# Optimization experiments

Hardware: AMD Instinct MI355X
Metric: run time of the kernel (lower is better)

The kernel has to match this reference:

```python
import jax, jax.numpy as jnp
import numpy as np
from jax import lax

EPS = 1e-6
D_MODEL = 2048
N_HEADS = 32
D_STATE = 64
HEADDIM = D_MODEL // N_HEADS  # 64, d_inner = expand*d_model = 2048
D_CONV = 4
INTER = 5504


def rmsnorm(x, w, eps=EPS):
    v = jnp.mean(jnp.square(x.astype(jnp.float32)), axis=-1, keepdims=True)
    return (x.astype(jnp.float32) * lax.rsqrt(v + eps)).astype(x.dtype) * w


def ssm_scan(x, dt, Bm, Cm):
    # x: (b,l,h,p) unscaled; dt: (b,l,h); Bm,Cm: (b,l,h,n)
    # DiscreteMamba2: h_t = exp(-dt_t) h_{t-1} + x_t (x) B_t ; y_t = h_t . C_t
    # (mamba_chunk_scan is called with x/dt and A=-1, so dt*(x/dt)=x)
    a = jnp.exp(-dt)  # (b,l,h)
    b, l, h, p = x.shape
    n = Bm.shape[-1]

    def step(hst, inp):
        a_t, x_t, B_t, C_t = inp
        hst = a_t[..., None, None] * hst + jnp.einsum('bhp,bhn->bhpn', x_t, B_t)
        y = jnp.einsum('bhpn,bhn->bhp', hst, C_t)
        return hst, y

    h0 = jnp.zeros((b, h, p, n), dtype=x.dtype)
    xs = (jnp.moveaxis(a, 1, 0), jnp.moveaxis(x, 1, 0),
          jnp.moveaxis(Bm, 1, 0), jnp.moveaxis(Cm, 1, 0))
    _, ys = lax.scan(step, h0, xs)
    return jnp.moveaxis(ys, 0, 1)  # (b,l,h,p)


def setup_inputs() -> dict:
    key = jax.random.key(0)
    ks = jax.random.split(key, 8)
    s = 0.02
    d_inner = D_MODEL
    conv_dim = d_inner + 2 * N_HEADS * D_STATE  # 6144
    d_in_proj = 2 * d_inner + 2 * N_HEADS * D_STATE + N_HEADS  # 8224
    return {
        'hidden_states': jax.random.normal(ks[0], (2, 2048, D_MODEL), jnp.float32),
        'attention_mask': jnp.ones((2, 2048), jnp.float32),
        'in_proj_w': jax.random.normal(ks[1], (d_in_proj, D_MODEL), jnp.float32) * s,
        'conv_w': jax.random.normal(ks[2], (conv_dim, 1, D_CONV), jnp.float32) * s,
        'conv_b': jnp.zeros((conv_dim,), jnp.float32),
        'z_bias': jnp.zeros((d_inner,), jnp.float32),
        'D': jnp.ones((N_HEADS,), jnp.float32),
        'out_proj_w': jax.random.normal(ks[3], (D_MODEL, d_inner), jnp.float32) * s,
        'ln1_w': jnp.ones((D_MODEL,), jnp.float32),
        'ln2_w': jnp.ones((D_MODEL,), jnp.float32),
        'gate_w': jax.random.normal(ks[4], (INTER, D_MODEL), jnp.float32) * s,
        'up_w': jax.random.normal(ks[5], (INTER, D_MODEL), jnp.float32) * s,
        'down_w': jax.random.normal(ks[6], (D_MODEL, INTER), jnp.float32) * s,
    }


def reference(hidden_states, attention_mask, in_proj_w, conv_w, conv_b, z_bias,
              D, out_proj_w, ln1_w, ln2_w, gate_w, up_w, down_w):
    b, l, d_model = hidden_states.shape
    d_inner = z_bias.shape[0]
    h_heads = D.shape[0]
    conv_dim = conv_w.shape[0]
    d_state = (conv_dim - d_inner) // (2 * h_heads)
    headdim = d_inner // h_heads

    residual = hidden_states
    h = rmsnorm(hidden_states, ln1_w)
    h = h * attention_mask[..., None]

    # --- DiscreteMamba2 mixer ---
    zxbcdt = jnp.einsum('bld,ed->ble', h, in_proj_w)
    z = zxbcdt[..., :d_inner]
    xBC = zxbcdt[..., d_inner:d_inner + conv_dim]
    A_log = zxbcdt[..., d_inner + conv_dim:]  # (b,l,h)

    # causal depthwise conv (activation = identity)
    xc = jnp.pad(jnp.swapaxes(xBC, 1, 2), ((0, 0), (0, 0), (conv_w.shape[-1] - 1, 0)))
    xBC = lax.conv_general_dilated(xc, conv_w, (1,), 'VALID',
                                   dimension_numbers=('NCH', 'OIH', 'NCH'),
                                   feature_group_count=conv_dim)
    xBC = jnp.swapaxes(xBC + conv_b[None, :, None], 1, 2)  # (b,l,conv_dim)

    x = xBC[..., :d_inner].reshape(b, l, h_heads, headdim)
    Bm = xBC[..., d_inner:d_inner + h_heads * d_state].reshape(b, l, h_heads, d_state)
    Cm = xBC[..., d_inner + h_heads * d_state:].reshape(b, l, h_heads, d_state)

    dt = jax.nn.softplus(A_log)  # (b,l,h)
    y = ssm_scan(x, dt, Bm, Cm)
    y = y + D[None, None, :, None] * x  # D skip uses unscaled x
    y = y.reshape(b, l, d_inner)

    gated = y * jax.nn.silu(z + z_bias)
    mixer_out = jnp.einsum('bld,ed->ble', gated, out_proj_w)

    h = mixer_out + residual
    residual2 = h
    h = rmsnorm(h, ln2_w)
    mlp = jnp.einsum('bli,di->bld',
                     jax.nn.silu(jnp.einsum('bld,id->bli', h, gate_w)) *
                     jnp.einsum('bld,id->bli', h, up_w),
                     down_w)
    return residual2 + mlp
```

## Files before the change

kernel.cpp:

```cpp
#include <hip/hip_runtime.h>
#include <math.h>

typedef __bf16 bf16_t;
typedef __attribute__((ext_vector_type(8))) __bf16 bf16x8;
typedef __attribute__((ext_vector_type(4))) float f32x4;

#define D_MODEL   2048
#define L_SEQ     2048
#define BATCH     2
#define NTOK      4096
#define N_HEADS   32
#define D_STATE   64
#define HEADDIM   64
#define D_INNER   2048
#define CONV_DIM  6144
#define D_IN_PROJ 8224
#define INTER     5504
#define QCHUNK    128
#define KCHUNKS   16

__device__ __forceinline__ void gld_lds16(const void* g, void* l) {
    __builtin_amdgcn_global_load_lds(
        (const __attribute__((address_space(1))) unsigned int*)g,
        (__attribute__((address_space(3))) unsigned int*)l, 16, 0, 0);
}

__device__ __forceinline__ int xcd_swizzle(int orig, int nwg) {
    int qx = nwg >> 3, rx = nwg & 7;
    int xcd = orig & 7, l8 = orig >> 3;
    return (xcd < rx ? xcd * (qx + 1) : rx * (qx + 1) + (xcd - rx) * qx) + l8;
}

__global__ __launch_bounds__(256) void cvt_kernel(
    const float* __restrict__ s, bf16_t* __restrict__ d, int n8)
{
    int i = blockIdx.x * 256 + threadIdx.x;
    if (i >= n8) return;
    const float4* s4 = (const float4*)s;
    float4 a = s4[2 * i], b = s4[2 * i + 1];
    bf16x8 r;
    r[0] = (bf16_t)a.x; r[1] = (bf16_t)a.y; r[2] = (bf16_t)a.z; r[3] = (bf16_t)a.w;
    r[4] = (bf16_t)b.x; r[5] = (bf16_t)b.y; r[6] = (bf16_t)b.z; r[7] = (bf16_t)b.w;
    ((bf16x8*)d)[i] = r;
}

__global__ __launch_bounds__(256) void rmsnorm_kernel(
    const float* __restrict__ x, const float* __restrict__ w,
    const float* __restrict__ mask, bf16_t* __restrict__ out)
{
    __shared__ float red[4];
    __shared__ float sinv;
    int row = blockIdx.x;
    const float* xr = x + (size_t)row * D_MODEL;
    float xv[8];
    float ss = 0.f;
#pragma unroll
    for (int i = 0; i < 8; ++i) {
        float v = xr[threadIdx.x + 256 * i];
        xv[i] = v;
        ss += v * v;
    }
    for (int off = 32; off >= 1; off >>= 1) ss += __shfl_down(ss, off, 64);
    int lane = threadIdx.x & 63, wv = threadIdx.x >> 6;
    if (lane == 0) red[wv] = ss;
    __syncthreads();
    if (threadIdx.x == 0) {
        float t = red[0] + red[1] + red[2] + red[3];
        sinv = rsqrtf(t / (float)D_MODEL + 1e-6f);
    }
    __syncthreads();
    float s = sinv;
    float m = mask ? mask[row] : 1.f;
    bf16_t* orow = out + (size_t)row * D_MODEL;
#pragma unroll
    for (int i = 0; i < 8; ++i) {
        int c = threadIdx.x + 256 * i;
        orow[c] = (bf16_t)(xv[i] * s * w[c] * m);
    }
}

template <bool RES, typename OT>
__global__ __launch_bounds__(256) void gemm_bt(
    const bf16_t* __restrict__ X, const bf16_t* __restrict__ W,
    const float* __restrict__ R, OT* __restrict__ O,
    int N, int K, int ldo)
{
    __shared__ __attribute__((aligned(16))) bf16_t As[128 * 32];
    __shared__ __attribute__((aligned(16))) bf16_t Bs[128 * 32];

    int tid = threadIdx.x;
    int ny = gridDim.y;
    int wg = xcd_swizzle(blockIdx.x + gridDim.x * blockIdx.y, gridDim.x * ny);
    int m0 = (wg % ny) * 128;
    int n0 = (wg / ny) * 128;

    f32x4 acc[4][4] = {};

    int lane = tid & 63;
    int wv = tid >> 6;
    int wm = (wv >> 1) * 64, wn = (wv & 1) * 64;
    int lm = lane & 15, lq = lane >> 4;

    int srow = tid >> 2;
    int scol = (tid & 3) * 8;
    const bf16_t* Xp0 = X + (size_t)(m0 + srow) * K + scol;
    const bf16_t* Xp1 = X + (size_t)(m0 + 64 + srow) * K + scol;
    int wr0 = n0 + srow;      if (wr0 > N - 1) wr0 = N - 1;
    int wr1 = n0 + 64 + srow; if (wr1 > N - 1) wr1 = N - 1;
    const bf16_t* Wp0 = W + (size_t)wr0 * K + scol;
    const bf16_t* Wp1 = W + (size_t)wr1 * K + scol;
    bf16_t* lA0 = &As[tid * 8];
    bf16_t* lA1 = &As[2048 + tid * 8];
    bf16_t* lB0 = &Bs[tid * 8];
    bf16_t* lB1 = &Bs[2048 + tid * 8];

    for (int k0 = 0; k0 < K; k0 += 32) {
        __syncthreads();
        gld_lds16(Xp0 + k0, lA0);
        gld_lds16(Xp1 + k0, lA1);
        gld_lds16(Wp0 + k0, lB0);
        gld_lds16(Wp1 + k0, lB1);
        __syncthreads();

        bf16x8 a[4], b[4];
#pragma unroll
        for (int i = 0; i < 4; ++i)
            a[i] = *(const bf16x8*)&As[(wm + i * 16 + lm) * 32 + lq * 8];
#pragma unroll
        for (int i = 0; i < 4; ++i)
            b[i] = *(const bf16x8*)&Bs[(wn + i * 16 + lm) * 32 + lq * 8];
#pragma unroll
        for (int mi = 0; mi < 4; ++mi)
#pragma unroll
            for (int ni = 0; ni < 4; ++ni)
                acc[mi][ni] = __builtin_amdgcn_mfma_f32_16x16x32_bf16(
                    a[mi], b[ni], acc[mi][ni], 0, 0, 0);
    }

#pragma unroll
    for (int mi = 0; mi < 4; ++mi)
#pragma unroll
        for (int ni = 0; ni < 4; ++ni) {
            int n = n0 + wn + ni * 16 + lm;
            if (n >= N) continue;
            int mbase = m0 + wm + mi * 16 + lq * 4;
#pragma unroll
            for (int r = 0; r < 4; ++r) {
                size_t off = (size_t)(mbase + r) * ldo + n;
                float v = acc[mi][ni][r];
                if (RES) v += R[off];
                O[off] = (OT)v;
            }
        }
}


#define G8_BARRIER() do { asm volatile("" ::: "memory"); \
    __builtin_amdgcn_s_barrier(); \
    asm volatile("" ::: "memory"); } while (0)
#define G8_LGKM0() do { asm volatile("s_waitcnt lgkmcnt(0)" ::: "memory"); \
    __builtin_amdgcn_sched_barrier(0); } while (0)
#define G8_VMCNT(n) asm volatile("s_waitcnt vmcnt(" #n ")" ::: "memory")

template <int W>
__device__ __forceinline__ void g8_stage(
    int tile, int NT, const bf16_t* pA, size_t hK64,
    const bf16_t* pB0, const bf16_t* pB1, const bf16_t* pB2, const bf16_t* pB3,
    unsigned dbase, bf16_t* lds)
{
    if (tile >= NT) return;
    unsigned so = ((tile & 1) ? 65536u : 0u) + (unsigned)W * 16384u;
    size_t goff = (size_t)tile * 64;
    const bf16_t *g0, *g1;
    if constexpr (W == 0)      { g0 = pA;              g1 = pA + hK64; }
    else if constexpr (W == 1) { g0 = pA + 2 * hK64;   g1 = pA + 3 * hK64; }
    else if constexpr (W == 2) { g0 = pB0;             g1 = pB1; }
    else                       { g0 = pB2;             g1 = pB3; }
    gld_lds16(g0 + goff, (char*)lds + (so + dbase));
    gld_lds16(g1 + goff, (char*)lds + (so + 8192u + dbase));
}

template <bool RES, typename OT>
__global__ __launch_bounds__(512, 2) void gemm8p(
    const bf16_t* __restrict__ X, const bf16_t* __restrict__ W,
    const float* __restrict__ R, OT* __restrict__ O,
    int N, int K, int ldo)
{
    __shared__ __attribute__((aligned(1024))) bf16_t lds[65536];

    const int tid  = threadIdx.x;
    const int lane = tid & 63;
    const int wid  = tid >> 6;
    const int wr   = wid >> 2;
    const int wc   = wid & 3;

    int ny = gridDim.y;
    int wg = xcd_swizzle(blockIdx.x + gridDim.x * blockIdx.y, gridDim.x * ny);
    int m0 = (wg % ny) * 256;
    int n0 = (wg / ny) * 256;

    const int NT    = K >> 6;
    const int niter = NT >> 1;

    int lrow = ((tid >> 7) << 4) + ((tid >> 2) & 15);
    int cb   = (tid & 3) * 16;
    int cblg = cb ^ (((tid >> 2) & 8) ? 32 : 0);
    int lcol = (((tid >> 6) & 1) << 5) + (cblg >> 1);
    const size_t hK64 = (size_t)K << 6;
    const bf16_t* pA = X + (size_t)(m0 + lrow) * K + lcol;
    const bf16_t* pB[4];
#pragma unroll
    for (int hi = 0; hi < 4; ++hi) {
        int rw = n0 + (hi >> 1) * 128 + (hi & 1) * 64 + lrow;
        if (rw > N - 1) rw = N - 1;
        pB[hi] = W + (size_t)rw * K + lcol;
    }
    const unsigned dbase = (unsigned)tid * 16u;

    unsigned c2s = ((unsigned)(lane >> 4) << 4) ^ ((lane & 8) ? 32u : 0u);
    unsigned rdA = (unsigned)(wr * 16384 + (lane & 15) * 64) + c2s;
    unsigned rdB = 32768u + (unsigned)((wc >> 1) * 16384 + (wc & 1) * 8192
                                       + (lane & 15) * 64) + c2s;

    f32x4 acc[8][4] = {};
    bf16x8 a[4][2], b[4][2];

#define G8_STG(W_, TILE) g8_stage<W_>((TILE), NT, pA, hK64, \
    pB[0], pB[1], pB[2], pB[3], dbase, lds)
#define G8_LDA(SO, HI) do { \
    const char* pa_ = (const char*)lds + (SO) + rdA + (HI) * 8192; \
    _Pragma("unroll") for (int mi = 0; mi < 4; ++mi) { \
        a[mi][0] = *(const bf16x8*)(pa_ + mi * 2048); \
        a[mi][1] = *(const bf16x8*)(pa_ + mi * 2048 + 1024); } \
} while (0)
#define G8_LDB(SO, NI0) do { \
    const char* pb_ = (const char*)lds + (SO) + rdB + (NI0) * 2048; \
    _Pragma("unroll") for (int nj = 0; nj < 2; ++nj) { \
        b[(NI0) + nj][0] = *(const bf16x8*)(pb_ + nj * 2048); \
        b[(NI0) + nj][1] = *(const bf16x8*)(pb_ + nj * 2048 + 1024); } \
} while (0)
#define G8_MFMAQ(MI0, NI0) do { \
    __builtin_amdgcn_s_setprio(1); \
    _Pragma("unroll") for (int mi = 0; mi < 4; ++mi) \
    _Pragma("unroll") for (int ni = 0; ni < 2; ++ni) \
    _Pragma("unroll") for (int ks = 0; ks < 2; ++ks) \
        acc[(MI0) + mi][(NI0) + ni] = __builtin_amdgcn_mfma_f32_16x16x32_bf16( \
            a[mi][ks], b[(NI0) + ni][ks], acc[(MI0) + mi][(NI0) + ni], 0, 0, 0); \
    __builtin_amdgcn_s_setprio(0); \
} while (0)

    G8_STG(2, 0); G8_STG(3, 0); G8_STG(0, 0); G8_STG(1, 0);
    G8_STG(2, 1); G8_STG(3, 1);
    G8_VMCNT(4);
    G8_BARRIER();

#pragma unroll 1
    for (int t = 0; t < niter; ++t) {
        const int t2 = 2 * t;
        G8_STG(0, t2 + 1);
        G8_LDA(0u, 0); G8_LDB(0u, 0);
        G8_BARRIER(); G8_LGKM0();
        G8_MFMAQ(0, 0);
        G8_BARRIER();
        G8_STG(1, t2 + 1);
        G8_LDB(0u, 2);
        G8_BARRIER(); G8_LGKM0();
        G8_MFMAQ(0, 2);
        G8_BARRIER();
        G8_STG(2, t2 + 2);
        G8_LDA(0u, 1);
        G8_BARRIER(); G8_LGKM0();
        G8_MFMAQ(4, 0);
        G8_BARRIER();
        G8_STG(3, t2 + 2);
        if (t == niter - 1) { G8_VMCNT(0); } else { G8_VMCNT(4); }
        G8_BARRIER();
        G8_MFMAQ(4, 2);
        G8_BARRIER();
        G8_STG(0, t2 + 2);
        G8_LDA(65536u, 0); G8_LDB(65536u, 0);
        G8_BARRIER(); G8_LGKM0();
        G8_MFMAQ(0, 0);
        G8_BARRIER();
        G8_STG(1, t2 + 2);
        G8_LDB(65536u, 2);
        G8_BARRIER(); G8_LGKM0();
        G8_MFMAQ(0, 2);
        G8_BARRIER();
        G8_STG(2, t2 + 3);
        G8_LDA(65536u, 1);
        G8_BARRIER(); G8_LGKM0();
        G8_MFMAQ(4, 0);
        G8_BARRIER();
        G8_STG(3, t2 + 3);
        G8_VMCNT(4);
        G8_BARRIER();
        G8_MFMAQ(4, 2);
        G8_BARRIER();
    }

#undef G8_STG
#undef G8_LDA
#undef G8_LDB
#undef G8_MFMAQ

#pragma unroll
    for (int mi = 0; mi < 8; ++mi)
#pragma unroll
        for (int ni = 0; ni < 4; ++ni) {
            int n = n0 + wc * 64 + ni * 16 + (lane & 15);
            if (n >= N) continue;
            int mbase = m0 + wr * 128 + mi * 16 + (lane >> 4) * 4;
#pragma unroll
            for (int r = 0; r < 4; ++r) {
                size_t off = (size_t)(mbase + r) * ldo + n;
                float v = acc[mi][ni][r];
                if (RES) v += R[off];
                O[off] = (OT)v;
            }
        }
}

__global__ __launch_bounds__(256) void conv_kernel(
    const bf16_t* __restrict__ zx, const float* __restrict__ cw,
    const float* __restrict__ cb, bf16_t* __restrict__ out)
{
    int c = blockIdx.x * 256 + threadIdx.x;
    int l0 = blockIdx.y * 128;
    int b = blockIdx.z;
    float w0 = cw[c * 4 + 0], w1 = cw[c * 4 + 1];
    float w2 = cw[c * 4 + 2], w3 = cw[c * 4 + 3];
    float bias = cb[c];
    const bf16_t* src = zx + (size_t)b * L_SEQ * D_IN_PROJ + 2048 + c;
    bf16_t* dst = out + (size_t)b * L_SEQ * CONV_DIM + c;
    float xm3 = (l0 >= 3) ? (float)src[(size_t)(l0 - 3) * D_IN_PROJ] : 0.f;
    float xm2 = (l0 >= 2) ? (float)src[(size_t)(l0 - 2) * D_IN_PROJ] : 0.f;
    float xm1 = (l0 >= 1) ? (float)src[(size_t)(l0 - 1) * D_IN_PROJ] : 0.f;
    for (int l = l0; l < l0 + 128; ++l) {
        float xc = (float)src[(size_t)l * D_IN_PROJ];
        float r = bias + xm3 * w0 + xm2 * w1 + xm1 * w2 + xc * w3;
        dst[(size_t)l * CONV_DIM] = (bf16_t)r;
        xm3 = xm2; xm2 = xm1; xm1 = xc;
    }
}

__global__ __launch_bounds__(256) void scan_state_kernel(
    const bf16_t* __restrict__ conv, const bf16_t* __restrict__ zx,
    float* __restrict__ Schunk, float* __restrict__ Aprod)
{
    const int SS = 32;
    __shared__ __attribute__((aligned(16))) float xs[SS][64];
    __shared__ __attribute__((aligned(16))) float bs[SS][64];
    __shared__ float as_[SS];

    int k = blockIdx.x, h = blockIdx.y, b = blockIdx.z;
    int tid = threadIdx.x, lane = tid & 63, wv = tid >> 6;
    int pt = tid >> 3, nt = tid & 7;
    int p0 = pt * 2, n0 = nt * 8;

    float st0[8] = {0, 0, 0, 0, 0, 0, 0, 0};
    float st1[8] = {0, 0, 0, 0, 0, 0, 0, 0};
    float aprod = 1.f;

    const bf16_t* cbase = conv + (size_t)b * L_SEQ * CONV_DIM + h * 64;
    const bf16_t* abase = zx + (size_t)b * L_SEQ * D_IN_PROJ + 8192 + h;

    int tstart = k * QCHUNK;
    for (int t0 = tstart; t0 < tstart + QCHUNK; t0 += SS) {
        int soff = (wv >> 1) * 16;
        for (int s = 0; s < 16; ++s) {
            size_t row = (size_t)(t0 + soff + s);
            if ((wv & 1) == 0) xs[soff + s][lane] = (float)cbase[row * CONV_DIM + lane];
            else               bs[soff + s][lane] = (float)cbase[row * CONV_DIM + 2048 + lane];
        }
        if (tid < SS) {
            float v = (float)abase[(size_t)(t0 + tid) * D_IN_PROJ];
            as_[tid] = 1.f / (1.f + __expf(v));
        }
        __syncthreads();
        for (int s = 0; s < SS; ++s) {
            float a = as_[s];
            float x0 = xs[s][p0], x1 = xs[s][p0 + 1];
            aprod *= a;
#pragma unroll
            for (int j = 0; j < 8; ++j) {
                float Bv = bs[s][n0 + j];
                st0[j] = a * st0[j] + x0 * Bv;
                st1[j] = a * st1[j] + x1 * Bv;
            }
        }
        __syncthreads();
    }
    size_t base = (((size_t)(b * N_HEADS + h)) * KCHUNKS + k) * 4096;
    float4* d0 = (float4*)&Schunk[base + p0 * 64 + n0];
    d0[0] = make_float4(st0[0], st0[1], st0[2], st0[3]);
    d0[1] = make_float4(st0[4], st0[5], st0[6], st0[7]);
    float4* d1 = (float4*)&Schunk[base + (p0 + 1) * 64 + n0];
    d1[0] = make_float4(st1[0], st1[1], st1[2], st1[3]);
    d1[1] = make_float4(st1[4], st1[5], st1[6], st1[7]);
    if (tid == 0) Aprod[(b * N_HEADS + h) * KCHUNKS + k] = aprod;
}

__global__ __launch_bounds__(256) void scan_combine_kernel(
    const float* __restrict__ Schunk, const float* __restrict__ Aprod,
    float* __restrict__ Sinit)
{
    int bh = blockIdx.x >> 4;
    int e = (blockIdx.x & 15) * 256 + threadIdx.x;
    size_t base = (size_t)bh * KCHUNKS * 4096 + e;
    float S = 0.f;
    for (int k = 0; k < KCHUNKS; ++k) {
        Sinit[base + (size_t)k * 4096] = S;
        float ap = Aprod[bh * KCHUNKS + k];
        S = ap * S + Schunk[base + (size_t)k * 4096];
    }
}

__global__ __launch_bounds__(256) void scan_out_kernel(
    const bf16_t* __restrict__ conv, const bf16_t* __restrict__ zx,
    const float* __restrict__ Sinit, const float* __restrict__ Dp,
    const float* __restrict__ zb, bf16_t* __restrict__ gated)
{
    const int S = 16;
    __shared__ __attribute__((aligned(16))) float xs[S][64];
    __shared__ __attribute__((aligned(16))) float bs[S][64];
    __shared__ __attribute__((aligned(16))) float cs[S][64];
    __shared__ __attribute__((aligned(16))) float zs[S][64];
    __shared__ float as_[S];

    int k = blockIdx.x, h = blockIdx.y, b = blockIdx.z;
    int tid = threadIdx.x;
    int lane = tid & 63, wv = tid >> 6;
    int pt = tid >> 3, nt = tid & 7;
    int p0 = pt * 2, n0 = nt * 8;

    size_t sbase = (((size_t)(b * N_HEADS + h)) * KCHUNKS + k) * 4096;
    float4 v00 = *(const float4*)&Sinit[sbase + p0 * 64 + n0];
    float4 v01 = *(const float4*)&Sinit[sbase + p0 * 64 + n0 + 4];
    float4 v10 = *(const float4*)&Sinit[sbase + (p0 + 1) * 64 + n0];
    float4 v11 = *(const float4*)&Sinit[sbase + (p0 + 1) * 64 + n0 + 4];
    float st0[8] = {v00.x, v00.y, v00.z, v00.w, v01.x, v01.y, v01.z, v01.w};
    float st1[8] = {v10.x, v10.y, v10.z, v10.w, v11.x, v11.y, v11.z, v11.w};

    float Dh  = Dp[h];
    float zb0 = zb[h * 64 + p0];
    float zb1 = zb[h * 64 + p0 + 1];

    const bf16_t* cbase = conv + (size_t)b * L_SEQ * CONV_DIM + h * 64;
    const bf16_t* zbase = zx + (size_t)b * L_SEQ * D_IN_PROJ + h * 64;
    const bf16_t* abase = zx + (size_t)b * L_SEQ * D_IN_PROJ + 8192 + h;
    bf16_t* obase = gated + (size_t)b * L_SEQ * D_INNER + h * 64;

    int tstart = k * QCHUNK;
    for (int t0 = tstart; t0 < tstart + QCHUNK; t0 += S) {
        for (int s = 0; s < S; ++s) {
            size_t row = (size_t)(t0 + s);
            if (wv == 0)      xs[s][lane] = (float)cbase[row * CONV_DIM + lane];
            else if (wv == 1) bs[s][lane] = (float)cbase[row * CONV_DIM + 2048 + lane];
            else if (wv == 2) cs[s][lane] = (float)cbase[row * CONV_DIM + 4096 + lane];
            else              zs[s][lane] = (float)zbase[row * D_IN_PROJ + lane];
        }
        if (tid < S) {
            float v = (float)abase[(size_t)(t0 + tid) * D_IN_PROJ];
            as_[tid] = 1.f / (1.f + __expf(v));
        }
        __syncthreads();

        for (int s = 0; s < S; ++s) {
            float a = as_[s];
            float x0 = xs[s][p0], x1 = xs[s][p0 + 1];
            float part0 = 0.f, part1 = 0.f;
#pragma unroll
            for (int j = 0; j < 8; ++j) {
                float Bv = bs[s][n0 + j];
                float Cv = cs[s][n0 + j];
                st0[j] = a * st0[j] + x0 * Bv;
                st1[j] = a * st1[j] + x1 * Bv;
                part0 += st0[j] * Cv;
                part1 += st1[j] * Cv;
            }
            for (int o = 1; o < 8; o <<= 1) {
                part0 += __shfl_xor(part0, o, 64);
                part1 += __shfl_xor(part1, o, 64);
            }
            if (nt == 0) {
                float y0 = part0 + Dh * x0;
                float y1 = part1 + Dh * x1;
                float z0 = zs[s][p0] + zb0;
                float z1 = zs[s][p0 + 1] + zb1;
                y0 *= z0 / (1.f + __expf(-z0));
                y1 *= z1 / (1.f + __expf(-z1));
                bf16_t* o2 = obase + (size_t)(t0 + s) * D_INNER + p0;
                o2[0] = (bf16_t)y0;
                o2[1] = (bf16_t)y1;
            }
        }
        __syncthreads();
    }
}

__global__ __launch_bounds__(256) void act_kernel(
    const bf16_t* __restrict__ gu, bf16_t* __restrict__ act, int n8)
{
    int i = blockIdx.x * 256 + threadIdx.x;
    if (i >= n8) return;
    int row = i / (INTER / 8);
    int c8  = i % (INTER / 8);
    const bf16x8* g = (const bf16x8*)(gu + (size_t)row * (2 * INTER)) + c8;
    const bf16x8* u = (const bf16x8*)(gu + (size_t)row * (2 * INTER) + INTER) + c8;
    bf16x8 gv = *g, uv = *u, r;
#pragma unroll
    for (int j = 0; j < 8; ++j) {
        float x = (float)gv[j];
        r[j] = (bf16_t)((x / (1.f + __expf(-x))) * (float)uv[j]);
    }
    ((bf16x8*)act)[i] = r;
}

extern "C" void kernel_launch(void* const* d_in, const int* in_sizes, int n_in,
                              void* d_out, int out_size, void* d_ws, size_t ws_size,
                              hipStream_t stream) {
    const float* hidden     = (const float*)d_in[0];
    const float* mask       = (const float*)d_in[1];
    const float* in_proj_w  = (const float*)d_in[2];
    const float* conv_w     = (const float*)d_in[3];
    const float* conv_b     = (const float*)d_in[4];
    const float* z_bias     = (const float*)d_in[5];
    const float* Dvec       = (const float*)d_in[6];
    const float* out_proj_w = (const float*)d_in[7];
    const float* ln1_w      = (const float*)d_in[8];
    const float* ln2_w      = (const float*)d_in[9];
    const float* gate_w     = (const float*)d_in[10];
    const float* up_w       = (const float*)d_in[11];
    const float* down_w     = (const float*)d_in[12];
    float* out = (float*)d_out;

    char* ws = (char*)d_ws;
    bf16_t* zxb    = (bf16_t*)(ws + 0);
    bf16_t* convo  = (bf16_t*)(ws + 67371008);
    bf16_t* hn     = (bf16_t*)(ws + 117702656);
    bf16_t* gated  = (bf16_t*)(ws + 117702656);
    float*  Schunk = (float*) (ws + 134479872);
    bf16_t* wbuf   = (bf16_t*)(ws + 151257088);
    float*  Sinit  = (float*) (ws + 151257088);
    float*  Aprod  = (float*) (ws + 168034304);
    bf16_t* guO    = (bf16_t*)(ws + 0);
    bf16_t* guW    = (bf16_t*)(ws + 90177536);
    bf16_t* actO   = (bf16_t*)(ws + 90177536);
    bf16_t* h2n    = (bf16_t*)(ws + 135266304);
    bf16_t* dwW    = (bf16_t*)(ws + 135266304);

    rmsnorm_kernel<<<NTOK, 256, 0, stream>>>(hidden, ln1_w, mask, hn);
    cvt_kernel<<<8224, 256, 0, stream>>>(in_proj_w, wbuf, D_IN_PROJ * D_MODEL / 8);
    gemm8p<false, bf16_t><<<dim3(32, 16), 512, 0, stream>>>(
        hn, wbuf, nullptr, zxb, 8192, D_MODEL, D_IN_PROJ);
    gemm_bt<false, bf16_t><<<dim3(1, 32), 256, 0, stream>>>(
        hn, wbuf + (size_t)8192 * D_MODEL, nullptr, zxb + 8192, 32, D_MODEL, D_IN_PROJ);
    conv_kernel<<<dim3(24, 16, 2), 256, 0, stream>>>(zxb, conv_w, conv_b, convo);
    scan_state_kernel<<<dim3(KCHUNKS, N_HEADS, BATCH), 256, 0, stream>>>(convo, zxb, Schunk, Aprod);
    scan_combine_kernel<<<1024, 256, 0, stream>>>(Schunk, Aprod, Sinit);
    scan_out_kernel<<<dim3(KCHUNKS, N_HEADS, BATCH), 256, 0, stream>>>(convo, zxb, Sinit, Dvec, z_bias, gated);
    cvt_kernel<<<2048, 256, 0, stream>>>(out_proj_w, wbuf, D_MODEL * D_INNER / 8);
    gemm_bt<true, float><<<dim3(16, 32), 256, 0, stream>>>(
        gated, wbuf, hidden, out, D_MODEL, D_INNER, D_MODEL);
    rmsnorm_kernel<<<NTOK, 256, 0, stream>>>(out, ln2_w, nullptr, h2n);
    cvt_kernel<<<5504, 256, 0, stream>>>(gate_w, guW, INTER * D_MODEL / 8);
    cvt_kernel<<<5504, 256, 0, stream>>>(up_w, guW + (size_t)INTER * D_MODEL, INTER * D_MODEL / 8);
    gemm8p<false, bf16_t><<<dim3(43, 16), 512, 0, stream>>>(
        h2n, guW, nullptr, guO, 2 * INTER, D_MODEL, 2 * INTER);
    act_kernel<<<11008, 256, 0, stream>>>(guO, actO, NTOK * INTER / 8);
    cvt_kernel<<<5504, 256, 0, stream>>>(down_w, dwW, D_MODEL * INTER / 8);
    gemm_bt<true, float><<<dim3(16, 32), 256, 0, stream>>>(
        actO, dwW, out, out, D_MODEL, INTER, D_MODEL);
}
```

Measured before the change: 1.040 ms.

## Software-pipeline LDS fragment loads one phase ahead of MFMA in gemm8p

Restructures the 8-wave GEMM main loop so LDS reads for the next MFMA quarter are issued before the current quarter's MFMAs. It drops the explicit lgkmcnt(0) waits and doubles the A fragment registers so both halves stay resident. It also collapses the four B row pointers into one base plus stride and removes the N-bound clamp and store guard. The aim is to hide LDS latency behind matrix math, at the cost of more VGPRs and no safety for N not a multiple of the tile (e.g. D_IN_PROJ 8224).

```diff
diff --git a/kernel.cpp b/kernel.cpp
--- a/kernel.cpp
+++ b/kernel.cpp
@@ -158,14 +158,12 @@
 #define G8_BARRIER() do { asm volatile("" ::: "memory"); \
     __builtin_amdgcn_s_barrier(); \
     asm volatile("" ::: "memory"); } while (0)
-#define G8_LGKM0() do { asm volatile("s_waitcnt lgkmcnt(0)" ::: "memory"); \
-    __builtin_amdgcn_sched_barrier(0); } while (0)
 #define G8_VMCNT(n) asm volatile("s_waitcnt vmcnt(" #n ")" ::: "memory")
+#define G8_SCHED() __builtin_amdgcn_sched_barrier(0)
 
 template <int W>
 __device__ __forceinline__ void g8_stage(
-    int tile, int NT, const bf16_t* pA, size_t hK64,
-    const bf16_t* pB0, const bf16_t* pB1, const bf16_t* pB2, const bf16_t* pB3,
+    int tile, int NT, const bf16_t* pA, const bf16_t* pB, size_t hK64,
     unsigned dbase, bf16_t* lds)
 {
     if (tile >= NT) return;
@@ -174,8 +172,8 @@
     const bf16_t *g0, *g1;
     if constexpr (W == 0)      { g0 = pA;              g1 = pA + hK64; }
     else if constexpr (W == 1) { g0 = pA + 2 * hK64;   g1 = pA + 3 * hK64; }
-    else if constexpr (W == 2) { g0 = pB0;             g1 = pB1; }
-    else                       { g0 = pB2;             g1 = pB3; }
+    else if constexpr (W == 2) { g0 = pB;              g1 = pB + hK64; }
+    else                       { g0 = pB + 2 * hK64;   g1 = pB + 3 * hK64; }
     gld_lds16(g0 + goff, (char*)lds + (so + dbase));
     gld_lds16(g1 + goff, (char*)lds + (so + 8192u + dbase));
 }
@@ -208,13 +206,7 @@
     int lcol = (((tid >> 6) & 1) << 5) + (cblg >> 1);
     const size_t hK64 = (size_t)K << 6;
     const bf16_t* pA = X + (size_t)(m0 + lrow) * K + lcol;
-    const bf16_t* pB[4];
-#pragma unroll
-    for (int hi = 0; hi < 4; ++hi) {
-        int rw = n0 + (hi >> 1) * 128 + (hi & 1) * 64 + lrow;
-        if (rw > N - 1) rw = N - 1;
-        pB[hi] = W + (size_t)rw * K + lcol;
-    }
+    const bf16_t* pB = W + (size_t)(n0 + lrow) * K + lcol;
     const unsigned dbase = (unsigned)tid * 16u;
 
     unsigned c2s = ((unsigned)(lane >> 4) << 4) ^ ((lane & 8) ? 32u : 0u);
@@ -223,15 +215,14 @@
                                        + (lane & 15) * 64) + c2s;
 
     f32x4 acc[8][4] = {};
-    bf16x8 a[4][2], b[4][2];
-
-#define G8_STG(W_, TILE) g8_stage<W_>((TILE), NT, pA, hK64, \
-    pB[0], pB[1], pB[2], pB[3], dbase, lds)
+    bf16x8 a[8][2], b[4][2];
+
+#define G8_STG(W_, TILE) g8_stage<W_>((TILE), NT, pA, pB, hK64, dbase, lds)
 #define G8_LDA(SO, HI) do { \
     const char* pa_ = (const char*)lds + (SO) + rdA + (HI) * 8192; \
     _Pragma("unroll") for (int mi = 0; mi < 4; ++mi) { \
-        a[mi][0] = *(const bf16x8*)(pa_ + mi * 2048); \
-        a[mi][1] = *(const bf16x8*)(pa_ + mi * 2048 + 1024); } \
+        a[(HI) * 4 + mi][0] = *(const bf16x8*)(pa_ + mi * 2048); \
+        a[(HI) * 4 + mi][1] = *(const bf16x8*)(pa_ + mi * 2048 + 1024); } \
 } while (0)
 #define G8_LDB(SO, NI0) do { \
     const char* pb_ = (const char*)lds + (SO) + rdB + (NI0) * 2048; \
@@ -245,7 +236,7 @@
     _Pragma("unroll") for (int ni = 0; ni < 2; ++ni) \
     _Pragma("unroll") for (int ks = 0; ks < 2; ++ks) \
         acc[(MI0) + mi][(NI0) + ni] = __builtin_amdgcn_mfma_f32_16x16x32_bf16( \
-            a[mi][ks], b[(NI0) + ni][ks], acc[(MI0) + mi][(NI0) + ni], 0, 0, 0); \
+            a[(MI0) + mi][ks], b[(NI0) + ni][ks], acc[(MI0) + mi][(NI0) + ni], 0, 0, 0); \
     __builtin_amdgcn_s_setprio(0); \
 } while (0)
 
@@ -253,48 +244,51 @@
     G8_STG(2, 1); G8_STG(3, 1);
     G8_VMCNT(4);
     G8_BARRIER();
+    G8_LDA(0u, 0); G8_LDB(0u, 0);
 
 #pragma unroll 1
     for (int t = 0; t < niter; ++t) {
         const int t2 = 2 * t;
         G8_STG(0, t2 + 1);
-        G8_LDA(0u, 0); G8_LDB(0u, 0);
-        G8_BARRIER(); G8_LGKM0();
+        G8_LDB(0u, 2);
+        G8_BARRIER(); G8_SCHED();
         G8_MFMAQ(0, 0);
         G8_BARRIER();
         G8_STG(1, t2 + 1);
-        G8_LDB(0u, 2);
-        G8_BARRIER(); G8_LGKM0();
+        G8_LDA(0u, 1);
+        G8_BARRIER(); G8_SCHED();
         G8_MFMAQ(0, 2);
         G8_BARRIER();
         G8_STG(2, t2 + 2);
-        G8_LDA(0u, 1);
-        G8_BARRIER(); G8_LGKM0();
+        G8_BARRIER(); G8_SCHED();
         G8_MFMAQ(4, 0);
         G8_BARRIER();
         G8_STG(3, t2 + 2);
         if (t == niter - 1) { G8_VMCNT(0); } else { G8_VMCNT(4); }
         G8_BARRIER();
+        G8_LDA(65536u, 0); G8_LDB(65536u, 0);
+        G8_SCHED();
         G8_MFMAQ(4, 2);
         G8_BARRIER();
         G8_STG(0, t2 + 2);
-        G8_LDA(65536u, 0); G8_LDB(65536u, 0);
-        G8_BARRIER(); G8_LGKM0();
+        G8_LDB(65536u, 2);
+        G8_BARRIER(); G8_SCHED();
         G8_MFMAQ(0, 0);
         G8_BARRIER();
         G8_STG(1, t2 + 2);
-        G8_LDB(65536u, 2);
-        G8_BARRIER(); G8_LGKM0();
+        G8_LDA(65536u, 1);
+        G8_BARRIER(); G8_SCHED();
         G8_MFMAQ(0, 2);
         G8_BARRIER();
         G8_STG(2, t2 + 3);
-        G8_LDA(65536u, 1);
-        G8_BARRIER(); G8_LGKM0();
+        G8_BARRIER(); G8_SCHED();
         G8_MFMAQ(4, 0);
         G8_BARRIER();
         G8_STG(3, t2 + 3);
         G8_VMCNT(4);
         G8_BARRIER();
+        if (t < niter - 1) { G8_LDA(0u, 0); G8_LDB(0u, 0); }
+        G8_SCHED();
         G8_MFMAQ(4, 2);
         G8_BARRIER();
     }
@@ -309,7 +303,6 @@
 #pragma unroll
         for (int ni = 0; ni < 4; ++ni) {
             int n = n0 + wc * 64 + ni * 16 + (lane & 15);
-            if (n >= N) continue;
             int mbase = m0 + wr * 128 + mi * 16 + (lane >> 4) * 4;
 #pragma unroll
             for (int r = 0; r < 4; ++r) {
```

Measured after the change: 1.169 ms. +12.4%, slower.

## Merge GEMM pipeline phases into half-tile MFMA blocks and drop N clamping

Applied to the files above, without the earlier changes.

Restructures the main GEMM loop so each k-tile runs two phases of 4x4 MFMAs instead of four quarter phases. That halves the barriers and LDS-wait points per tile. Global-to-LDS stages are issued in pairs, and B-row pointers are now derived from a single base pointer. The clamp on B rows past N and the store bound check are removed. This is only safe if the weight and output buffers are padded to a multiple of 256 rows, since N values such as 8224 and 5504 are not.

```diff
diff --git a/kernel.cpp b/kernel.cpp
--- a/kernel.cpp
+++ b/kernel.cpp
@@ -164,8 +164,7 @@
 
 template <int W>
 __device__ __forceinline__ void g8_stage(
-    int tile, int NT, const bf16_t* pA, size_t hK64,
-    const bf16_t* pB0, const bf16_t* pB1, const bf16_t* pB2, const bf16_t* pB3,
+    int tile, int NT, const bf16_t* pA, const bf16_t* pB, size_t hK64,
     unsigned dbase, bf16_t* lds)
 {
     if (tile >= NT) return;
@@ -174,8 +173,8 @@
     const bf16_t *g0, *g1;
     if constexpr (W == 0)      { g0 = pA;              g1 = pA + hK64; }
     else if constexpr (W == 1) { g0 = pA + 2 * hK64;   g1 = pA + 3 * hK64; }
-    else if constexpr (W == 2) { g0 = pB0;             g1 = pB1; }
-    else                       { g0 = pB2;             g1 = pB3; }
+    else if constexpr (W == 2) { g0 = pB;              g1 = pB + hK64; }
+    else                       { g0 = pB + 2 * hK64;   g1 = pB + 3 * hK64; }
     gld_lds16(g0 + goff, (char*)lds + (so + dbase));
     gld_lds16(g1 + goff, (char*)lds + (so + 8192u + dbase));
 }
@@ -208,13 +207,7 @@
     int lcol = (((tid >> 6) & 1) << 5) + (cblg >> 1);
     const size_t hK64 = (size_t)K << 6;
     const bf16_t* pA = X + (size_t)(m0 + lrow) * K + lcol;
-    const bf16_t* pB[4];
-#pragma unroll
-    for (int hi = 0; hi < 4; ++hi) {
-        int rw = n0 + (hi >> 1) * 128 + (hi & 1) * 64 + lrow;
-        if (rw > N - 1) rw = N - 1;
-        pB[hi] = W + (size_t)rw * K + lcol;
-    }
+    const bf16_t* pB = W + (size_t)(n0 + lrow) * K + lcol;
     const unsigned dbase = (unsigned)tid * 16u;
 
     unsigned c2s = ((unsigned)(lane >> 4) << 4) ^ ((lane & 8) ? 32u : 0u);
@@ -225,8 +218,7 @@
     f32x4 acc[8][4] = {};
     bf16x8 a[4][2], b[4][2];
 
-#define G8_STG(W_, TILE) g8_stage<W_>((TILE), NT, pA, hK64, \
-    pB[0], pB[1], pB[2], pB[3], dbase, lds)
+#define G8_STG(W_, TILE) g8_stage<W_>((TILE), NT, pA, pB, hK64, dbase, lds)
 #define G8_LDA(SO, HI) do { \
     const char* pa_ = (const char*)lds + (SO) + rdA + (HI) * 8192; \
     _Pragma("unroll") for (int mi = 0; mi < 4; ++mi) { \
@@ -239,17 +231,17 @@
         b[(NI0) + nj][0] = *(const bf16x8*)(pb_ + nj * 2048); \
         b[(NI0) + nj][1] = *(const bf16x8*)(pb_ + nj * 2048 + 1024); } \
 } while (0)
-#define G8_MFMAQ(MI0, NI0) do { \
+#define G8_MFMAH(MI0) do { \
     __builtin_amdgcn_s_setprio(1); \
     _Pragma("unroll") for (int mi = 0; mi < 4; ++mi) \
-    _Pragma("unroll") for (int ni = 0; ni < 2; ++ni) \
+    _Pragma("unroll") for (int ni = 0; ni < 4; ++ni) \
     _Pragma("unroll") for (int ks = 0; ks < 2; ++ks) \
-        acc[(MI0) + mi][(NI0) + ni] = __builtin_amdgcn_mfma_f32_16x16x32_bf16( \
-            a[mi][ks], b[(NI0) + ni][ks], acc[(MI0) + mi][(NI0) + ni], 0, 0, 0); \
+        acc[(MI0) + mi][ni] = __builtin_amdgcn_mfma_f32_16x16x32_bf16( \
+            a[mi][ks], b[ni][ks], acc[(MI0) + mi][ni], 0, 0, 0); \
     __builtin_amdgcn_s_setprio(0); \
 } while (0)
 
-    G8_STG(2, 0); G8_STG(3, 0); G8_STG(0, 0); G8_STG(1, 0);
+    G8_STG(0, 0); G8_STG(1, 0); G8_STG(2, 0); G8_STG(3, 0);
     G8_STG(2, 1); G8_STG(3, 1);
     G8_VMCNT(4);
     G8_BARRIER();
@@ -257,59 +249,40 @@
 #pragma unroll 1
     for (int t = 0; t < niter; ++t) {
         const int t2 = 2 * t;
-        G8_STG(0, t2 + 1);
-        G8_LDA(0u, 0); G8_LDB(0u, 0);
+        G8_STG(0, t2 + 1); G8_STG(1, t2 + 1);
+        G8_LDA(0u, 0); G8_LDB(0u, 0); G8_LDB(0u, 2);
         G8_BARRIER(); G8_LGKM0();
-        G8_MFMAQ(0, 0);
+        G8_MFMAH(0);
         G8_BARRIER();
-        G8_STG(1, t2 + 1);
-        G8_LDB(0u, 2);
+        G8_STG(2, t2 + 2); G8_STG(3, t2 + 2);
+        G8_LDA(0u, 1);
+        if (t == niter - 1) { G8_VMCNT(0); } else { G8_VMCNT(4); }
         G8_BARRIER(); G8_LGKM0();
-        G8_MFMAQ(0, 2);
+        G8_MFMAH(4);
         G8_BARRIER();
-        G8_STG(2, t2 + 2);
-        G8_LDA(0u, 1);
+        G8_STG(0, t2 + 2); G8_STG(1, t2 + 2);
+        G8_LDA(65536u, 0); G8_LDB(65536u, 0); G8_LDB(65536u, 2);
         G8_BARRIER(); G8_LGKM0();
-        G8_MFMAQ(4, 0);
+        G8_MFMAH(0);
         G8_BARRIER();
-        G8_STG(3, t2 + 2);
-        if (t == niter - 1) { G8_VMCNT(0); } else { G8_VMCNT(4); }
-        G8_BARRIER();
-        G8_MFMAQ(4, 2);
-        G8_BARRIER();
-        G8_STG(0, t2 + 2);
-        G8_LDA(65536u, 0); G8_LDB(65536u, 0);
+        G8_STG(2, t2 + 3); G8_STG(3, t2 + 3);
+        G8_LDA(65536u, 1);
+        G8_VMCNT(4);
         G8_BARRIER(); G8_LGKM0();
-        G8_MFMAQ(0, 0);
-        G8_BARRIER();
-        G8_STG(1, t2 + 2);
-        G8_LDB(65536u, 2);
-        G8_BARRIER(); G8_LGKM0();
-        G8_MFMAQ(0, 2);
-        G8_BARRIER();
-        G8_STG(2, t2 + 3);
-        G8_LDA(65536u, 1);
-        G8_BARRIER(); G8_LGKM0();
-        G8_MFMAQ(4, 0);
-        G8_BARRIER();
-        G8_STG(3, t2 + 3);
-        G8_VMCNT(4);
-        G8_BARRIER();
-        G8_MFMAQ(4, 2);
+        G8_MFMAH(4);
         G8_BARRIER();
     }
 
 #undef G8_STG
 #undef G8_LDA
 #undef G8_LDB
-#undef G8_MFMAQ
+#undef G8_MFMAH
 
 #pragma unroll
     for (int mi = 0; mi < 8; ++mi)
 #pragma unroll
         for (int ni = 0; ni < 4; ++ni) {
             int n = n0 + wc * 64 + ni * 16 + (lane & 15);
-            if (n >= N) continue;
             int mbase = m0 + wr * 128 + mi * 16 + (lane >> 4) * 4;
 #pragma unroll
             for (int r = 0; r < 4; ++r) {
```

Result: no change. 1.050 ms (+1.0%).
